# Performance work log

Measured on AMD Instinct MI355X. Metric: run time of the kernel, lower is better.

Reference implementation:

```python
import jax, jax.numpy as jnp
import numpy as np
from jax import lax

K_LOCAL = 8
CHUNK = 1024


def _local_features(template, surf_xyz, point_feat):
    # template: (B,T,3), surf_xyz: (B,S,3), point_feat: (B,S,D)
    B, T, _ = template.shape
    _, S, D = point_feat.shape
    n_chunks = T // CHUNK  # T chosen divisible by CHUNK
    tmpl = template.reshape(B, n_chunks, CHUNK, 3).transpose(1, 0, 2, 3)  # (n_chunks,B,c,3)
    s_sq = jnp.sum(surf_xyz * surf_xyz, axis=-1)  # (B,S)

    def body(carry, t):  # t: (B,c,3)
        t_sq = jnp.sum(t * t, axis=-1)  # (B,c)
        # squared distances; monotone in true distance so top-k indices match cdist
        d2 = t_sq[..., None] + s_sq[:, None, :] - 2.0 * jnp.einsum('bcd,bsd->bcs', t, surf_xyz)
        _, idx = lax.top_k(-d2, K_LOCAL)  # (B,c,k) nearest
        flat = idx.reshape(B, -1)  # (B,c*k)
        g = jnp.take_along_axis(point_feat, flat[..., None], axis=1)  # (B,c*k,D)
        local = g.reshape(B, CHUNK, K_LOCAL, D).mean(axis=2)  # (B,c,D)
        return carry, local

    _, locals_ = lax.scan(body, None, tmpl)  # (n_chunks,B,c,D)
    return locals_.transpose(1, 0, 2, 3).reshape(B, T, D)


def setup_inputs() -> dict:
    key = jax.random.key(0)
    ks = jax.random.split(key, 12)
    B, T, S, D, G = 4, 16384, 8192, 256, 512
    inp_dim, H = 3 + D + G, 256
    w = lambda k, sh: (jax.random.normal(k, sh, dtype=jnp.float32) * 0.02)
    return {
        'template': jax.random.normal(ks[0], (B, T, 3), dtype=jnp.float32),
        'surf_xyz': jax.random.normal(ks[1], (B, S, 3), dtype=jnp.float32),
        'global_feat': jax.random.normal(ks[2], (B, G), dtype=jnp.float32),
        'point_feat': jax.random.normal(ks[3], (B, S, D), dtype=jnp.float32),
        'dw1': w(ks[4], (inp_dim, H)), 'db1': jnp.zeros((H,), jnp.float32),
        'dw2': w(ks[5], (H, H)), 'db2': jnp.zeros((H,), jnp.float32),
        'dw3': w(ks[6], (H, 3)), 'db3': jnp.zeros((3,), jnp.float32),
        'mw1': w(ks[7], (inp_dim, H // 2)), 'mb1': jnp.zeros((H // 2,), jnp.float32),
        'mw2': w(ks[8], (H // 2, 64)), 'mb2': jnp.zeros((64,), jnp.float32),
        'mw3': w(ks[9], (64, 1)), 'mb3': jnp.zeros((1,), jnp.float32),
    }


def reference(template, surf_xyz, global_feat, point_feat,
              dw1, db1, dw2, db2, dw3, db3,
              mw1, mb1, mw2, mb2, mw3, mb3):
    B, T, _ = template.shape
    local = _local_features(template, surf_xyz, point_feat)  # (B,T,256)
    g = jnp.broadcast_to(global_feat[:, None, :], (B, T, global_feat.shape[-1]))
    x = jnp.concatenate([template, local, g], axis=-1)  # (B,T,771)
    # disp head (dropout = identity in eval)
    h = jax.nn.relu(x @ dw1 + db1)
    h = jax.nn.relu(h @ dw2 + db2)
    disp = h @ dw3 + db3  # (B,T,3)
    # material head
    m = jax.nn.relu(x @ mw1 + mb1)
    m = jax.nn.relu(m @ mw2 + mb2)
    mat = jax.nn.sigmoid(m @ mw3 + mb3)[..., 0]  # (B,T)
    return disp, mat
```

## Files before the change

### kernel.cpp

```cpp
#include <hip/hip_runtime.h>
#include <cstdint>


#define T_PTS 16384
#define S_PTS 8192
#define B_SZ 4
#define D_FEAT 256
#define G_FEAT 512
#define M_ROWS (B_SZ * T_PTS)
#define K1 320
#define N1 384
#define DISP_SZ (M_ROWS * 3)
#define NCHUNK 4
#define CHUNK_S (S_PTS / NCHUNK)
#define NPLANE (NCHUNK * 8)
#define NCELL 32768

using u16 = unsigned short;
typedef short bf16x8 __attribute__((ext_vector_type(8)));
typedef float f32x4 __attribute__((ext_vector_type(4)));

__device__ __forceinline__ u16 f2bf(float f) {
  uint32_t x = __builtin_bit_cast(uint32_t, f);
  x += 0x7fffu + ((x >> 16) & 1u);
  return (u16)(x >> 16);
}
__device__ __forceinline__ float bf2f(u16 h) {
  uint32_t x = ((uint32_t)h) << 16;
  return __builtin_bit_cast(float, x);
}
__device__ __forceinline__ void gload16(void* lds, const void* g) {
  __builtin_amdgcn_global_load_lds(
      (const __attribute__((address_space(1))) unsigned int*)g,
      (__attribute__((address_space(3))) unsigned int*)lds, 16, 0, 0);
}


__global__ __launch_bounds__(256) void prep_surf(const float* __restrict__ sxyz,
                                                 float4* __restrict__ surfp) {
  int i = blockIdx.x * 256 + threadIdx.x;
  float x = sxyz[(size_t)i * 3], y = sxyz[(size_t)i * 3 + 1], z = sxyz[(size_t)i * 3 + 2];
  float4 v;
  v.x = x; v.y = y; v.z = z; v.w = fmaf(x, x, fmaf(y, y, z * z));
  surfp[i] = v;
}

__global__ __launch_bounds__(256) void prep_w(
    const float* __restrict__ dw1, const float* __restrict__ mw1,
    const float* __restrict__ dw2, const float* __restrict__ mw2,
    u16* __restrict__ w1t, u16* __restrict__ w2t, u16* __restrict__ w2bt) {
  int i = blockIdx.x * 256 + threadIdx.x;
  if (i < 122880) {
    int n = i / 320, k = i % 320;
    float v = 0.f;
    if (k < 256)      v = (n < 256) ? dw1[(size_t)(3 + k) * 256 + n] : mw1[(size_t)(3 + k) * 128 + (n - 256)];
    else if (k < 259) v = (n < 256) ? dw1[(size_t)(k - 256) * 256 + n] : mw1[(size_t)(k - 256) * 128 + (n - 256)];
    w1t[i] = f2bf(v);
  } else if (i < 188416) {
    int j = i - 122880;
    int n = j >> 8, k = j & 255;
    w2t[j] = f2bf(dw2[(size_t)k * 256 + n]);
  } else {
    int j = i - 188416;
    int n = j >> 7, k = j & 127;
    w2bt[j] = f2bf(mw2[(size_t)k * 64 + n]);
  }
}

__global__ __launch_bounds__(512) void bias1_k(
    const float* __restrict__ gf, const float* __restrict__ dw1,
    const float* __restrict__ mw1, const float* __restrict__ db1,
    const float* __restrict__ mb1, float* __restrict__ bias1) {
  __shared__ float red[512];
  int b = blockIdx.x, nc = blockIdx.y;
  int tn = threadIdx.x & 127, tk = threadIdx.x >> 7;
  int n = nc * 128 + tn;
  const float* g = gf + b * G_FEAT;
  float s = 0.f;
  if (n < 256) {
    for (int k = tk * 128; k < tk * 128 + 128; k++)
      s = fmaf(g[k], dw1[(size_t)(259 + k) * 256 + n], s);
  } else {
    for (int k = tk * 128; k < tk * 128 + 128; k++)
      s = fmaf(g[k], mw1[(size_t)(259 + k) * 128 + (n - 256)], s);
  }
  red[threadIdx.x] = s;
  __syncthreads();
  if (tk == 0) {
    float base = (n < 256) ? db1[n] : mb1[n - 256];
    bias1[b * N1 + n] = base + ((red[tn] + red[tn + 128]) + (red[tn + 256] + red[tn + 384]));
  }
}


__device__ __forceinline__ int spread5(int v) {
  return (v & 1) | ((v & 2) << 2) | ((v & 4) << 4) | ((v & 8) << 6) | ((v & 16) << 8);
}
__device__ __forceinline__ int morton15(float x, float y, float z) {
  int ix = (int)fminf(31.f, fmaxf(0.f, (x + 4.f) * 4.f));
  int iy = (int)fminf(31.f, fmaxf(0.f, (y + 4.f) * 4.f));
  int iz = (int)fminf(31.f, fmaxf(0.f, (z + 4.f) * 4.f));
  return (spread5(ix) << 2) | (spread5(iy) << 1) | spread5(iz);
}

__global__ __launch_bounds__(256) void zbins_k(int* __restrict__ bins) {
  bins[blockIdx.x * 256 + threadIdx.x] = 0;
}

__global__ __launch_bounds__(256) void hist_t_k(const float* __restrict__ tmpl,
                                                int* __restrict__ bins_t,
                                                int* __restrict__ cellb) {
  int i = blockIdx.x * 256 + threadIdx.x;
  int b = i >> 14;
  int c = morton15(tmpl[(size_t)i * 3], tmpl[(size_t)i * 3 + 1], tmpl[(size_t)i * 3 + 2]);
  cellb[i] = c;
  atomicAdd(&bins_t[b * NCELL + c], 1);
}

__global__ __launch_bounds__(1024) void scan1_k(int* __restrict__ bins,
                                                int* __restrict__ segsum) {
  __shared__ int sd[2048];
  int seg = blockIdx.x, tid = threadIdx.x;
  int* bb = bins + seg * 2048;
  int e0 = bb[2 * tid], e1 = bb[2 * tid + 1];
  sd[tid] = e0 + e1;
  __syncthreads();
  int cur = 0;
#pragma unroll
  for (int s = 0; s < 10; ++s) {
    int off = 1 << s;
    int val = sd[cur * 1024 + tid] + ((tid >= off) ? sd[cur * 1024 + tid - off] : 0);
    sd[(1 - cur) * 1024 + tid] = val;
    __syncthreads();
    cur ^= 1;
  }
  int incl = sd[cur * 1024 + tid];
  int excl = incl - (e0 + e1);
  bb[2 * tid] = excl;
  bb[2 * tid + 1] = excl + e0;
  if (tid == 1023) segsum[seg] = incl;
}

__global__ __launch_bounds__(64) void scan2_k(int* __restrict__ segsum) {
  __shared__ int tot[64];
  int tid = threadIdx.x;
  int b = tid >> 4, w = tid & 15;
  tot[tid] = segsum[tid];
  __syncthreads();
  int s = 0;
  for (int j = 0; j < 16; ++j) s += (j < w) ? tot[b * 16 + j] : 0;
  segsum[tid] = s;
}

__global__ __launch_bounds__(256) void scatter_t_k(const float* __restrict__ tmpl,
                                                   const int* __restrict__ cellb,
                                                   int* __restrict__ bins_t,
                                                   const int* __restrict__ segbase,
                                                   int* __restrict__ perm,
                                                   float4* __restrict__ tmplS) {
  int i = blockIdx.x * 256 + threadIdx.x;
  int b = i >> 14, t = i & 16383;
  int idx = b * NCELL + cellb[i];
  int local = atomicAdd(&bins_t[idx], 1);
  int dst = (b << 14) + segbase[idx >> 11] + local;
  perm[dst] = t;
  float4 v;
  v.x = tmpl[(size_t)i * 3]; v.y = tmpl[(size_t)i * 3 + 1]; v.z = tmpl[(size_t)i * 3 + 2];
  v.w = 0.f;
  tmplS[dst] = v;
}

__global__ __launch_bounds__(256) void knn_part_k(const float4* __restrict__ surfp,
                                                  const float4* __restrict__ tmplS,
                                                  float* __restrict__ part_d,
                                                  int* __restrict__ part_i) {
  const int ch = blockIdx.y, b = blockIdx.z;
  const int t = (blockIdx.x << 8) + threadIdx.x;
  const int gi = b * T_PTS + t;

  const float4* sp = surfp + (size_t)b * S_PTS + ch * CHUNK_S;

  float4 tp = tmplS[gi];
  float nx = -2.f * tp.x, ny = -2.f * tp.y, nz = -2.f * tp.z;
  float tsq = fmaf(tp.x, tp.x, fmaf(tp.y, tp.y, tp.z * tp.z));

  float dd[8]; int ii[8];
#pragma unroll
  for (int q = 0; q < 8; q++) { dd[q] = 3e38f; ii[q] = 0; }
  float worst = 3e38f;

  auto proc = [&](const float4* c, int base) {
    float d2[8];
#pragma unroll
    for (int q = 0; q < 8; q++)
      d2[q] = fmaf(nx, c[q].x, fmaf(ny, c[q].y, fmaf(nz, c[q].z, tsq + c[q].w)));
    float m = fminf(fminf(fminf(d2[0], d2[1]), fminf(d2[2], d2[3])),
                    fminf(fminf(d2[4], d2[5]), fminf(d2[6], d2[7])));
    if (m < worst) {
#pragma unroll
      for (int q = 0; q < 8; ++q) {
        float v = d2[q];
        if (v < worst) {
          int gx = base + q;
#pragma unroll
          for (int r = 7; r >= 1; --r) {
            bool cr = v < dd[r], cr1 = v < dd[r - 1];
            dd[r] = cr ? (cr1 ? dd[r - 1] : v) : dd[r];
            ii[r] = cr ? (cr1 ? ii[r - 1] : gx) : ii[r];
          }
          bool c0 = v < dd[0];
          dd[0] = c0 ? v : dd[0];
          ii[0] = c0 ? gx : ii[0];
          worst = dd[7];
        }
      }
    }
  };

  float4 ca[8], cb[8];
#pragma unroll
  for (int q = 0; q < 8; q++) ca[q] = sp[q];

  constexpr int NG = CHUNK_S / 8;
  for (int g = 0; g < NG; g += 2) {
#pragma unroll
    for (int q = 0; q < 8; q++) cb[q] = sp[(g + 1) * 8 + q];
    proc(ca, g * 8);
#pragma unroll
    for (int q = 0; q < 8; q++) ca[q] = sp[((g + 2) & (NG - 1)) * 8 + q];
    proc(cb, (g + 1) * 8);
  }

#pragma unroll
  for (int q = 0; q < 8; q++) {
    part_d[(size_t)(ch * 8 + q) * M_ROWS + gi] = dd[q];
    part_i[(size_t)(ch * 8 + q) * M_ROWS + gi] = ii[q] + ch * CHUNK_S;
  }
}

__global__ __launch_bounds__(256) void knn_merge_k(const float* __restrict__ part_d,
                                                   const int* __restrict__ part_i,
                                                   int* __restrict__ knn) {
  int pt = blockIdx.x * 256 + threadIdx.x;
  float d[NPLANE]; int x[NPLANE];
#pragma unroll
  for (int q = 0; q < NPLANE; q++) {
    d[q] = part_d[(size_t)q * M_ROWS + pt];
    x[q] = part_i[(size_t)q * M_ROWS + pt];
  }
#pragma unroll
  for (int s = 0; s < 8; s++) {
    float bd = d[0]; int bx = x[0]; int bp = 0;
#pragma unroll
    for (int q = 1; q < NPLANE; q++) {
      bool lt = (d[q] < bd) || (d[q] == bd && x[q] < bx);
      bd = lt ? d[q] : bd;
      bx = lt ? x[q] : bx;
      bp = lt ? q : bp;
    }
    knn[(size_t)pt * 8 + s] = bx;
#pragma unroll
    for (int q = 0; q < NPLANE; q++)
      if (q == bp) d[q] = 3e38f;
  }
}

__global__ __launch_bounds__(256) void gather_k(const int* __restrict__ knn,
                                                const float* __restrict__ pf,
                                                const float4* __restrict__ tmplS,
                                                u16* __restrict__ xb) {
  int m = blockIdx.x * 4 + (threadIdx.x >> 6);
  int lane = threadIdx.x & 63;
  int b = m >> 14;
  const int* id = knn + (size_t)m * 8;
  const float* base = pf + (size_t)b * S_PTS * D_FEAT;
  float ax = 0, ay = 0, az = 0, aw = 0;
#pragma unroll
  for (int k = 0; k < 8; k++) {
    const float4* p = (const float4*)(base + (size_t)id[k] * D_FEAT) + lane;
    float4 v = *p;
    ax += v.x; ay += v.y; az += v.z; aw += v.w;
  }
  ushort4 o;
  o.x = f2bf(ax * 0.125f); o.y = f2bf(ay * 0.125f);
  o.z = f2bf(az * 0.125f); o.w = f2bf(aw * 0.125f);
  *(ushort4*)(xb + (size_t)m * K1 + lane * 4) = o;
  float4 tp = tmplS[m];
  float tv = (lane == 0) ? tp.x : (lane == 1) ? tp.y : (lane == 2) ? tp.z : 0.f;
  xb[(size_t)m * K1 + 256 + lane] = f2bf(tv);
}

template <int BM, int BN>
__global__ __launch_bounds__(256) void gemm_k(const u16* __restrict__ X, int ldx,
                                              const u16* __restrict__ Wt,
                                              const float* __restrict__ bias, int bstride,
                                              u16* __restrict__ Y, int ldy, int K) {
  constexpr int WM = 2, WN = 2;
  constexpr int FM = BM / WM / 16, FN = BN / WN / 16;
  __shared__ u16 As[BM * 64];
  __shared__ u16 Bs[BN * 64];
  const int tid = threadIdx.x, lane = tid & 63, wid = tid >> 6;
  const int m0 = blockIdx.x * BM, n0 = blockIdx.y * BN;
  const int wm0 = (wid / WN) * (BM / WM), wn0 = (wid % WN) * (BN / WN);

  f32x4 acc[FM][FN] = {};

  for (int kt = 0; kt < K; kt += 64) {
#pragma unroll
    for (int i = 0; i < BM * 8 / 256; i++) {
      int c = i * 256 + tid;
      int r = c >> 3, s = c & 7;
      int ss = s ^ (r & 7);
      gload16(As + c * 8, X + (size_t)(m0 + r) * ldx + kt + ss * 8);
    }
#pragma unroll
    for (int i = 0; i < BN * 8 / 256; i++) {
      int c = i * 256 + tid;
      int r = c >> 3, s = c & 7;
      int ss = s ^ (r & 7);
      gload16(Bs + c * 8, Wt + (size_t)(n0 + r) * K + kt + ss * 8);
    }
    __syncthreads();
#pragma unroll
    for (int kk = 0; kk < 2; kk++) {
      bf16x8 af[FM], bfr[FN];
#pragma unroll
      for (int i = 0; i < FM; i++) {
        int r = wm0 + i * 16 + (lane & 15);
        int q = kk * 4 + (lane >> 4);
        af[i] = *(const bf16x8*)(As + r * 64 + ((q ^ (r & 7)) * 8));
      }
#pragma unroll
      for (int j = 0; j < FN; j++) {
        int r = wn0 + j * 16 + (lane & 15);
        int q = kk * 4 + (lane >> 4);
        bfr[j] = *(const bf16x8*)(Bs + r * 64 + ((q ^ (r & 7)) * 8));
      }
#pragma unroll
      for (int i = 0; i < FM; i++)
#pragma unroll
        for (int j = 0; j < FN; j++)
          acc[i][j] = __builtin_amdgcn_mfma_f32_16x16x32_bf16(af[i], bfr[j], acc[i][j], 0, 0, 0);
    }
    __syncthreads();
  }

  const float* brow = bias + (size_t)(m0 / T_PTS) * bstride;
#pragma unroll
  for (int i = 0; i < FM; i++)
#pragma unroll
    for (int j = 0; j < FN; j++)
#pragma unroll
      for (int r = 0; r < 4; r++) {
        int rl = wm0 + i * 16 + (lane >> 4) * 4 + r;
        int cl = wn0 + j * 16 + (lane & 15);
        float v = acc[i][j][r] + brow[n0 + cl];
        v = fmaxf(v, 0.f);
        Y[(size_t)(m0 + rl) * ldy + n0 + cl] = f2bf(v);
      }
}

__global__ __launch_bounds__(256) void final_k(const u16* __restrict__ h2,
                                               const u16* __restrict__ m2,
                                               const float* __restrict__ dw3,
                                               const float* __restrict__ db3,
                                               const float* __restrict__ mw3,
                                               const float* __restrict__ mb3,
                                               const int* __restrict__ perm,
                                               float* __restrict__ out) {
  int m = blockIdx.x * 4 + (threadIdx.x >> 6);
  int lane = threadIdx.x & 63;
  ushort4 hv = *(const ushort4*)(h2 + (size_t)m * 256 + lane * 4);
  float hq[4] = {bf2f(hv.x), bf2f(hv.y), bf2f(hv.z), bf2f(hv.w)};
  float a0 = 0, a1 = 0, a2 = 0, am = 0;
#pragma unroll
  for (int q = 0; q < 4; q++) {
    int k = lane * 4 + q;
    a0 = fmaf(hq[q], dw3[(size_t)k * 3 + 0], a0);
    a1 = fmaf(hq[q], dw3[(size_t)k * 3 + 1], a1);
    a2 = fmaf(hq[q], dw3[(size_t)k * 3 + 2], a2);
  }
  if (lane < 16) {
    ushort4 mv = *(const ushort4*)(m2 + (size_t)m * 64 + lane * 4);
    float mq[4] = {bf2f(mv.x), bf2f(mv.y), bf2f(mv.z), bf2f(mv.w)};
#pragma unroll
    for (int q = 0; q < 4; q++) am = fmaf(mq[q], mw3[lane * 4 + q], am);
  }
#pragma unroll
  for (int off = 32; off > 0; off >>= 1) {
    a0 += __shfl_down(a0, off);
    a1 += __shfl_down(a1, off);
    a2 += __shfl_down(a2, off);
    am += __shfl_down(am, off);
  }
  if (lane == 0) {
    int b = m >> 14;
    int orig = (b << 14) + perm[m];
    out[(size_t)orig * 3 + 0] = a0 + db3[0];
    out[(size_t)orig * 3 + 1] = a1 + db3[1];
    out[(size_t)orig * 3 + 2] = a2 + db3[2];
    float s = am + mb3[0];
    out[DISP_SZ + orig] = 1.f / (1.f + expf(-s));
  }
}


extern "C" void kernel_launch(void* const* d_in, const int* in_sizes, int n_in,
                              void* d_out, int out_size, void* d_ws, size_t ws_size,
                              hipStream_t stream) {
  const float* tmpl = (const float*)d_in[0];
  const float* sxyz = (const float*)d_in[1];
  const float* gf   = (const float*)d_in[2];
  const float* pf   = (const float*)d_in[3];
  const float* dw1  = (const float*)d_in[4];
  const float* db1  = (const float*)d_in[5];
  const float* dw2  = (const float*)d_in[6];
  const float* db2  = (const float*)d_in[7];
  const float* dw3  = (const float*)d_in[8];
  const float* db3  = (const float*)d_in[9];
  const float* mw1  = (const float*)d_in[10];
  const float* mb1  = (const float*)d_in[11];
  const float* mw2  = (const float*)d_in[12];
  const float* mb2  = (const float*)d_in[13];
  const float* mw3  = (const float*)d_in[14];
  const float* mb3  = (const float*)d_in[15];

  char* ws = (char*)d_ws;
  float4* surfp  = (float4*)(ws + 0);
  int*    knn    = (int*)(ws + 524288);
  u16*    xb     = (u16*)(ws + 2621440);
  float*  part_d = (float*)(ws + 2621440);
  int*    part_i = (int*)(ws + 11010048);
  u16*    w1t    = (u16*)(ws + 44564480);
  u16*    w2t    = (u16*)(ws + 44810240);
  u16*    w2bt   = (u16*)(ws + 44941312);
  float*  bias1  = (float*)(ws + 44957696);
  u16*    h1     = (u16*)(ws + 44963840);
  int*    cellb  = (int*)(ws + 44963840);
  int*    bins   = (int*)(ws + 45225984);
  int*    segsum = (int*)(ws + 45750272);
  float4* tmplS  = (float4*)(ws + 45750528);
  u16*    h2     = (u16*)(ws + 95295488);
  u16*    m2     = (u16*)(ws + 128849920);
  int*    perm   = (int*)(ws + 137238528);
  float*  out    = (float*)d_out;

  prep_surf<<<128, 256, 0, stream>>>(sxyz, surfp);
  prep_w<<<768, 256, 0, stream>>>(dw1, mw1, dw2, mw2, w1t, w2t, w2bt);
  bias1_k<<<dim3(B_SZ, 3), 512, 0, stream>>>(gf, dw1, mw1, db1, mb1, bias1);
  zbins_k<<<512, 256, 0, stream>>>(bins);
  hist_t_k<<<256, 256, 0, stream>>>(tmpl, bins, cellb);
  scan1_k<<<64, 1024, 0, stream>>>(bins, segsum);
  scan2_k<<<1, 64, 0, stream>>>(segsum);
  scatter_t_k<<<256, 256, 0, stream>>>(tmpl, cellb, bins, segsum, perm, tmplS);
  knn_part_k<<<dim3(64, NCHUNK, B_SZ), 256, 0, stream>>>(surfp, tmplS, part_d, part_i);
  knn_merge_k<<<256, 256, 0, stream>>>(part_d, part_i, knn);
  gather_k<<<16384, 256, 0, stream>>>(knn, pf, tmplS, xb);
  gemm_k<128, 128><<<dim3(512, 3), 256, 0, stream>>>(xb, K1, w1t, bias1, N1, h1, N1, K1);
  gemm_k<128, 128><<<dim3(512, 2), 256, 0, stream>>>(h1, N1, w2t, db2, 0, h2, 256, 256);
  gemm_k<128, 64><<<dim3(512, 1), 256, 0, stream>>>(h1 + 256, N1, w2bt, mb2, 0, m2, 64, 128);
  final_k<<<16384, 256, 0, stream>>>(h2, m2, dw3, db3, mw3, mb3, perm, out);
}
```

Before: 423.9 us.

## Project point features through first layer before gathering neighbours

Uses linearity of the mean and the first layer: each surface point's features are first multiplied by the first-layer weights (8192x4 rows, 384 cols) in a GEMM. Each template point then gathers and averages 8 projected rows, adding bias and template-xyz terms, to produce h1 directly. This replaces the large 65536x320 first-layer GEMM with a 32768x256 GEMM. The cost is a gather of 384-wide fp32 rows instead of 256-wide ones and an extra bf16 conversion pass over point_feat.

```diff
diff --git a/kernel.cpp b/kernel.cpp
--- a/kernel.cpp
+++ b/kernel.cpp
@@ -8,7 +8,6 @@
 #define D_FEAT 256
 #define G_FEAT 512
 #define M_ROWS (B_SZ * T_PTS)
-#define K1 320
 #define N1 384
 #define DISP_SZ (M_ROWS * 3)
 #define NCHUNK 4
@@ -45,23 +44,30 @@
   surfp[i] = v;
 }
 
+__global__ __launch_bounds__(256) void prep_pf(const float* __restrict__ pf,
+                                               u16* __restrict__ pfb) {
+  int i = blockIdx.x * 256 + threadIdx.x;
+  float4 v = ((const float4*)pf)[i];
+  ushort4 o;
+  o.x = f2bf(v.x); o.y = f2bf(v.y); o.z = f2bf(v.z); o.w = f2bf(v.w);
+  ((ushort4*)pfb)[i] = o;
+}
+
 __global__ __launch_bounds__(256) void prep_w(
     const float* __restrict__ dw1, const float* __restrict__ mw1,
     const float* __restrict__ dw2, const float* __restrict__ mw2,
-    u16* __restrict__ w1t, u16* __restrict__ w2t, u16* __restrict__ w2bt) {
+    u16* __restrict__ w1lt, u16* __restrict__ w2t, u16* __restrict__ w2bt) {
   int i = blockIdx.x * 256 + threadIdx.x;
-  if (i < 122880) {
-    int n = i / 320, k = i % 320;
-    float v = 0.f;
-    if (k < 256)      v = (n < 256) ? dw1[(size_t)(3 + k) * 256 + n] : mw1[(size_t)(3 + k) * 128 + (n - 256)];
-    else if (k < 259) v = (n < 256) ? dw1[(size_t)(k - 256) * 256 + n] : mw1[(size_t)(k - 256) * 128 + (n - 256)];
-    w1t[i] = f2bf(v);
-  } else if (i < 188416) {
-    int j = i - 122880;
+  if (i < 98304) {
+    int n = i >> 8, k = i & 255;
+    float v = (n < 256) ? dw1[(size_t)(3 + k) * 256 + n] : mw1[(size_t)(3 + k) * 128 + (n - 256)];
+    w1lt[i] = f2bf(v);
+  } else if (i < 163840) {
+    int j = i - 98304;
     int n = j >> 8, k = j & 255;
     w2t[j] = f2bf(dw2[(size_t)k * 256 + n]);
-  } else {
-    int j = i - 188416;
+  } else if (i < 172032) {
+    int j = i - 163840;
     int n = j >> 7, k = j & 127;
     w2bt[j] = f2bf(mw2[(size_t)k * 64 + n]);
   }
@@ -265,36 +271,50 @@
   }
 }
 
-__global__ __launch_bounds__(256) void gather_k(const int* __restrict__ knn,
-                                                const float* __restrict__ pf,
-                                                const float4* __restrict__ tmplS,
-                                                u16* __restrict__ xb) {
+__global__ __launch_bounds__(256) void gather_h1(const int* __restrict__ knn,
+                                                 const float* __restrict__ PW,
+                                                 const float* __restrict__ bias1,
+                                                 const float4* __restrict__ tmplS,
+                                                 const float* __restrict__ dw1,
+                                                 const float* __restrict__ mw1,
+                                                 u16* __restrict__ h1) {
   int m = blockIdx.x * 4 + (threadIdx.x >> 6);
   int lane = threadIdx.x & 63;
   int b = m >> 14;
   const int* id = knn + (size_t)m * 8;
-  const float* base = pf + (size_t)b * S_PTS * D_FEAT;
-  float ax = 0, ay = 0, az = 0, aw = 0;
+  const float* PWb = PW + (size_t)b * S_PTS * N1;
+  float acc[6] = {0.f, 0.f, 0.f, 0.f, 0.f, 0.f};
 #pragma unroll
   for (int k = 0; k < 8; k++) {
-    const float4* p = (const float4*)(base + (size_t)id[k] * D_FEAT) + lane;
-    float4 v = *p;
-    ax += v.x; ay += v.y; az += v.z; aw += v.w;
-  }
-  ushort4 o;
-  o.x = f2bf(ax * 0.125f); o.y = f2bf(ay * 0.125f);
-  o.z = f2bf(az * 0.125f); o.w = f2bf(aw * 0.125f);
-  *(ushort4*)(xb + (size_t)m * K1 + lane * 4) = o;
+    const float* pr = PWb + (size_t)id[k] * N1;
+#pragma unroll
+    for (int p = 0; p < 6; p++) acc[p] += pr[p * 64 + lane];
+  }
   float4 tp = tmplS[m];
-  float tv = (lane == 0) ? tp.x : (lane == 1) ? tp.y : (lane == 2) ? tp.z : 0.f;
-  xb[(size_t)m * K1 + 256 + lane] = f2bf(tv);
-}
-
-template <int BM, int BN>
+  const float* brow = bias1 + b * N1;
+#pragma unroll
+  for (int p = 0; p < 6; p++) {
+    int n = p * 64 + lane;
+    float w0, w1, w2;
+    if (p < 4) {
+      w0 = dw1[n]; w1 = dw1[256 + n]; w2 = dw1[512 + n];
+    } else {
+      int nm = n - 256;
+      w0 = mw1[nm]; w1 = mw1[128 + nm]; w2 = mw1[256 + nm];
+    }
+    float h = fmaf(acc[p], 0.125f, brow[n]);
+    h = fmaf(tp.x, w0, h);
+    h = fmaf(tp.y, w1, h);
+    h = fmaf(tp.z, w2, h);
+    h1[(size_t)m * N1 + n] = f2bf(fmaxf(h, 0.f));
+  }
+}
+
+template <int BM, int BN, bool RELU, bool BIAS, bool F32OUT>
 __global__ __launch_bounds__(256) void gemm_k(const u16* __restrict__ X, int ldx,
                                               const u16* __restrict__ Wt,
-                                              const float* __restrict__ bias, int bstride,
-                                              u16* __restrict__ Y, int ldy, int K) {
+                                              const float* __restrict__ bias,
+                                              void* __restrict__ Yv, int ldy, int K) {
   constexpr int WM = 2, WN = 2;
   constexpr int FM = BM / WM / 16, FN = BN / WN / 16;
   __shared__ u16 As[BM * 64];
@@ -345,7 +365,6 @@
     __syncthreads();
   }
 
-  const float* brow = bias + (size_t)(m0 / T_PTS) * bstride;
 #pragma unroll
   for (int i = 0; i < FM; i++)
 #pragma unroll
@@ -354,9 +373,13 @@
       for (int r = 0; r < 4; r++) {
         int rl = wm0 + i * 16 + (lane >> 4) * 4 + r;
         int cl = wn0 + j * 16 + (lane & 15);
-        float v = acc[i][j][r] + brow[n0 + cl];
-        v = fmaxf(v, 0.f);
-        Y[(size_t)(m0 + rl) * ldy + n0 + cl] = f2bf(v);
+        float v = acc[i][j][r];
+        if (BIAS) v += bias[n0 + cl];
+        if (RELU) v = fmaxf(v, 0.f);
+        if (F32OUT)
+          ((float*)Yv)[(size_t)(m0 + rl) * ldy + n0 + cl] = v;
+        else
+          ((u16*)Yv)[(size_t)(m0 + rl) * ldy + n0 + cl] = f2bf(v);
       }
 }
 
@@ -428,36 +451,41 @@
   char* ws = (char*)d_ws;
   float4* surfp  = (float4*)(ws + 0);
   int*    knn    = (int*)(ws + 524288);
-  u16*    xb     = (u16*)(ws + 2621440);
-  float*  part_d = (float*)(ws + 2621440);
-  int*    part_i = (int*)(ws + 11010048);
-  u16*    w1t    = (u16*)(ws + 44564480);
-  u16*    w2t    = (u16*)(ws + 44810240);
-  u16*    w2bt   = (u16*)(ws + 44941312);
-  float*  bias1  = (float*)(ws + 44957696);
-  u16*    h1     = (u16*)(ws + 44963840);
-  int*    cellb  = (int*)(ws + 44963840);
-  int*    bins   = (int*)(ws + 45225984);
-  int*    segsum = (int*)(ws + 45750272);
-  float4* tmplS  = (float4*)(ws + 45750528);
-  u16*    h2     = (u16*)(ws + 95295488);
-  u16*    m2     = (u16*)(ws + 128849920);
-  int*    perm   = (int*)(ws + 137238528);
+  float4* tmplS  = (float4*)(ws + 2621440);
+  int*    perm   = (int*)(ws + 3670016);
+  float*  bias1  = (float*)(ws + 3932160);
+  u16*    w1lt   = (u16*)(ws + 3938304);
+  u16*    w2t    = (u16*)(ws + 4134912);
+  u16*    w2bt   = (u16*)(ws + 4265984);
+  int*    cellb  = (int*)(ws + 4282368);
+  int*    bins   = (int*)(ws + 4544512);
+  int*    segsum = (int*)(ws + 5068800);
+  u16*    pfb    = (u16*)(ws + 5069056);
+  float*  PW     = (float*)(ws + 21846272);
+  u16*    h1     = (u16*)(ws + 72177920);
+  u16*    h2     = (u16*)(ws + 21846272);
+  u16*    m2     = (u16*)(ws + 55400704);
+  float*  part_d = (float*)(ws + 72177920);
+  int*    part_i = (int*)(ws + 80566528);
   float*  out    = (float*)d_out;
 
   prep_surf<<<128, 256, 0, stream>>>(sxyz, surfp);
-  prep_w<<<768, 256, 0, stream>>>(dw1, mw1, dw2, mw2, w1t, w2t, w2bt);
+  prep_pf<<<8192, 256, 0, stream>>>(pf, pfb);
+  prep_w<<<672, 256, 0, stream>>>(dw1, mw1, dw2, mw2, w1lt, w2t, w2bt);
   bias1_k<<<dim3(B_SZ, 3), 512, 0, stream>>>(gf, dw1, mw1, db1, mb1, bias1);
   zbins_k<<<512, 256, 0, stream>>>(bins);
   hist_t_k<<<256, 256, 0, stream>>>(tmpl, bins, cellb);
   scan1_k<<<64, 1024, 0, stream>>>(bins, segsum);
   scan2_k<<<1, 64, 0, stream>>>(segsum);
   scatter_t_k<<<256, 256, 0, stream>>>(tmpl, cellb, bins, segsum, perm, tmplS);
+  gemm_k<128, 128, false, false, true><<<dim3(256, 3), 256, 0, stream>>>(
+      pfb, 256, w1lt, nullptr, PW, N1, 256);
   knn_part_k<<<dim3(64, NCHUNK, B_SZ), 256, 0, stream>>>(surfp, tmplS, part_d, part_i);
   knn_merge_k<<<256, 256, 0, stream>>>(part_d, part_i, knn);
-  gather_k<<<16384, 256, 0, stream>>>(knn, pf, tmplS, xb);
-  gemm_k<128, 128><<<dim3(512, 3), 256, 0, stream>>>(xb, K1, w1t, bias1, N1, h1, N1, K1);
-  gemm_k<128, 128><<<dim3(512, 2), 256, 0, stream>>>(h1, N1, w2t, db2, 0, h2, 256, 256);
-  gemm_k<128, 64><<<dim3(512, 1), 256, 0, stream>>>(h1 + 256, N1, w2bt, mb2, 0, m2, 64, 128);
+  gather_h1<<<16384, 256, 0, stream>>>(knn, PW, bias1, tmplS, dw1, mw1, h1);
+  gemm_k<128, 128, true, true, false><<<dim3(512, 2), 256, 0, stream>>>(
+      h1, N1, w2t, db2, h2, 256, 256);
+  gemm_k<128, 64, true, true, false><<<dim3(512, 1), 256, 0, stream>>>(
+      h1 + 256, N1, w2bt, mb2, m2, 64, 128);
   final_k<<<16384, 256, 0, stream>>>(h2, m2, dw3, db3, mw3, mb3, perm, out);
 }
```

New measurement: 449.1 us. +5.9%, slower.
